# Optimization experiments

Hardware: AMD Instinct MI355X
Metric: run time of the kernel (lower is better)

The kernel has to match this reference:

```python
import jax, jax.numpy as jnp
import numpy as np

B, N, C, H, KH = 4, 4096, 1024, 16, 5
HD = C // H  # head dim = 64


def setup_inputs() -> dict:
    key = jax.random.key(0)
    ks = jax.random.split(key, 4)
    return {
        "x": jax.random.normal(ks[0], (B, N, C), jnp.float32),
        "qkv_w": jax.random.normal(ks[1], (3 * C, C), jnp.float32) * 0.02,
        "qkv_b": jnp.zeros((3 * C,), jnp.float32),
        "proj_w": jax.random.normal(ks[2], (C, C), jnp.float32) * 0.02,
        "proj_b": jnp.zeros((C,), jnp.float32),
        "pos_enc": jnp.zeros((1, C), jnp.float32),  # torch init: zeros
        "dwc_w": jax.random.normal(ks[3], (HD, 1, KH, KH), jnp.float32) * 0.05,
        "dwc_b": jnp.zeros((HD,), jnp.float32),
        "num_heads": H,
    }


def reference(x, qkv_w, qkv_b, proj_w, proj_b, pos_enc, dwc_w, dwc_b, num_heads):
    b, n, c = x.shape
    h = num_heads
    hd = c // h
    kh = dwc_w.shape[2]

    qkv = x @ qkv_w.T + qkv_b                     # (b, n, 3c)
    q, k, v = jnp.split(qkv, 3, axis=-1)          # each (b, n, c)
    k = k + pos_enc[:, :c]                        # broadcast (1, c)
    q = jax.nn.relu(q)
    k = jax.nn.relu(k)

    def to_heads(t):  # (b, n, c) -> (b*h, n, hd)
        return t.reshape(b, n, h, hd).transpose(0, 2, 1, 3).reshape(b * h, n, hd)

    q, k, v = to_heads(q), to_heads(k), to_heads(v)

    # linear attention in fp32 (inputs already fp32)
    z = 1.0 / (jnp.einsum('bic,bc->bi', q, k.sum(axis=1)) + 1e-6)   # (bh, n)
    kv = jnp.einsum('bjc,bjd->bcd', k, v)                           # (bh, hd, hd)
    out = jnp.einsum('bic,bcd->bid', q, kv) * z[:, :, None]         # (bh, n, hd)

    # depthwise 2D conv on v viewed as (bh, hd, n, 1), kernel (hd,1,kh,kh), pad kh//2
    fm = v.transpose(0, 2, 1)[..., None]                            # (bh, hd, n, 1)
    pad = kh // 2
    fm = jax.lax.conv_general_dilated(
        fm, dwc_w, window_strides=(1, 1),
        padding=((pad, pad), (pad, pad)),
        dimension_numbers=('NCHW', 'OIHW', 'NCHW'),
        feature_group_count=hd,
    ) + dwc_b[None, :, None, None]
    out = out + fm[..., 0].transpose(0, 2, 1)                       # (bh, n, hd)

    out = out.reshape(b, h, n, hd).transpose(0, 2, 1, 3).reshape(b, n, c)
    return out @ proj_w.T + proj_b
```

## Files before the change

### kernel.cpp

```cpp
#include <hip/hip_runtime.h>


#define BB   4
#define NN   4096
#define CDIM 1024
#define NH   16
#define HDIM 64
#define BH   64

typedef __attribute__((ext_vector_type(8))) short short8;
typedef __attribute__((ext_vector_type(4))) float f32x4;
typedef unsigned short u16;

__device__ __forceinline__ float b2f(short s) {
    union { unsigned u; float f; } c;
    c.u = ((unsigned)(unsigned short)s) << 16;
    return c.f;
}
__device__ __forceinline__ u16 f2b(float f) {
    unsigned u = __float_as_uint(f);
    return (u16)((u + 0x7fffu + ((u >> 16) & 1u)) >> 16);
}
__device__ __forceinline__ void gload16(const void* g, void* l) {
    __builtin_amdgcn_global_load_lds((const __attribute__((address_space(1))) void*)g,
                                     (__attribute__((address_space(3))) void*)l, 16, 0, 0);
}

__global__ __launch_bounds__(256) void k_fill_diag(float* __restrict__ out, int n, float val)
{
    int i = blockIdx.x * 256 + threadIdx.x;
    if (i < n) out[i] = val;
}

__global__ __launch_bounds__(256) void k_f32_to_bf16(const float* __restrict__ in,
                                                     u16* __restrict__ out, int n4)
{
    int i = blockIdx.x * 256 + threadIdx.x;
    if (i < n4) {
        float4 v = reinterpret_cast<const float4*>(in)[i];
        ushort4 o;
        o.x = f2b(v.x); o.y = f2b(v.y); o.z = f2b(v.z); o.w = f2b(v.w);
        reinterpret_cast<ushort4*>(out)[i] = o;
    }
}

#define GEMM256_8PH()                                                                    \
    const int t = threadIdx.x;                                                           \
    const int l = t & 63, w = t >> 6;                                                    \
    const int wr = w >> 2, wc = w & 3;                                                   \
    const int fr = l & 15;                                                               \
    const int physE  = ((l >> 4) ^ ((fr >> 1) & 3)) * 8;                                 \
    const int qa     = ((l & 3) ^ ((l >> 3) & 3)) * 8;                                   \
    const int aRow   = w * 16 + (l >> 2);                                                \
    const u16* gA0 = A  + (size_t)(brow + aRow) * 1024 + qa;                             \
    const u16* gB0 = Bw + (size_t)(bcol + aRow) * 1024 + qa;                             \
    char* ldsc = (char*)lds;                                                             \
    const int afBase = (wr * 128 + fr) * 32 + physE;                                     \
    const int bfBase = 16384 + (wc * 64 + fr) * 32 + physE;                              \
    f32x4 acc[8][4];                                                                     \
    _Pragma("unroll")                                                                    \
    for (int m = 0; m < 8; ++m)                                                          \
        _Pragma("unroll")                                                                \
        for (int n = 0; n < 4; ++n) acc[m][n] = (f32x4){0.f, 0.f, 0.f, 0.f};             \
    auto STG = [&](int kt, int kh, int isB) {                                            \
        const u16* g = (isB ? gB0 : gA0) + kt * 64 + kh * 32;                            \
        char* d = ldsc + (kt & 1) * 65536 + isB * 32768 + kh * 16384 + w * 1024 + l * 16;\
        gload16(g,          d);                                                          \
        gload16(g + 131072, d + 8192);                                                   \
    };                                                                                   \
    STG(0,0,0); STG(0,0,1); STG(0,1,0); STG(0,1,1); STG(1,0,0); STG(1,0,1);              \
    asm volatile("s_waitcnt vmcnt(4)" ::: "memory");                                     \
    __builtin_amdgcn_sched_barrier(0);                                                   \
    __builtin_amdgcn_s_barrier();                                                        \
    __builtin_amdgcn_sched_barrier(0);                                                   \
    _Pragma("unroll 1")                                                                  \
    for (int kt = 0; kt < 16; ++kt) {                                                    \
        const int B0 = (kt & 1) * 32768;                                                 \
        short8 af[4], bf[4];                                                             \
                                                               \
        _Pragma("unroll")                                                                \
        for (int m = 0; m < 4; ++m)                                                      \
            af[m] = *reinterpret_cast<const short8*>(&lds[B0 + afBase + m * 512]);       \
        _Pragma("unroll")                                                                \
        for (int n = 0; n < 4; ++n)                                                      \
            bf[n] = *reinterpret_cast<const short8*>(&lds[B0 + bfBase + n * 512]);       \
        if (kt + 1 < 16) STG(kt + 1, 1, 0);                                              \
        __builtin_amdgcn_sched_barrier(0);                                               \
        __builtin_amdgcn_s_barrier();                                                    \
        asm volatile("s_waitcnt lgkmcnt(0)" ::: "memory");                               \
        __builtin_amdgcn_sched_barrier(0);                                               \
        __builtin_amdgcn_s_setprio(1);                                                   \
        _Pragma("unroll")                                                                \
        for (int m = 0; m < 4; ++m)                                                      \
            _Pragma("unroll")                                                            \
            for (int n = 0; n < 4; ++n)                                                  \
                acc[m][n] = __builtin_amdgcn_mfma_f32_16x16x32_bf16(af[m], bf[n], acc[m][n], 0, 0, 0); \
        __builtin_amdgcn_s_setprio(0);                                                   \
        __builtin_amdgcn_sched_barrier(0);                                               \
        __builtin_amdgcn_s_barrier();                                                    \
        __builtin_amdgcn_sched_barrier(0);                                               \
                                                               \
        _Pragma("unroll")                                                                \
        for (int m = 0; m < 4; ++m)                                                      \
            af[m] = *reinterpret_cast<const short8*>(&lds[B0 + afBase + (m + 4) * 512]); \
        if (kt + 1 < 16) STG(kt + 1, 1, 1);                                              \
        __builtin_amdgcn_sched_barrier(0);                                               \
        __builtin_amdgcn_s_barrier();                                                    \
        asm volatile("s_waitcnt lgkmcnt(0)" ::: "memory");                               \
        __builtin_amdgcn_sched_barrier(0);                                               \
        __builtin_amdgcn_s_setprio(1);                                                   \
        _Pragma("unroll")                                                                \
        for (int m = 0; m < 4; ++m)                                                      \
            _Pragma("unroll")                                                            \
            for (int n = 0; n < 4; ++n)                                                  \
                acc[m + 4][n] = __builtin_amdgcn_mfma_f32_16x16x32_bf16(af[m], bf[n], acc[m + 4][n], 0, 0, 0); \
        __builtin_amdgcn_s_setprio(0);                                                   \
        __builtin_amdgcn_sched_barrier(0);                                               \
        __builtin_amdgcn_s_barrier();                                                    \
        __builtin_amdgcn_sched_barrier(0);                                               \
                                                               \
        _Pragma("unroll")                                                                \
        for (int m = 0; m < 4; ++m)                                                      \
            af[m] = *reinterpret_cast<const short8*>(&lds[B0 + 8192 + afBase + m * 512]);\
        _Pragma("unroll")                                                                \
        for (int n = 0; n < 4; ++n)                                                      \
            bf[n] = *reinterpret_cast<const short8*>(&lds[B0 + 8192 + bfBase + n * 512]);\
        if (kt + 2 < 16) STG(kt + 2, 0, 0);                                              \
        __builtin_amdgcn_sched_barrier(0);                                               \
        __builtin_amdgcn_s_barrier();                                                    \
        asm volatile("s_waitcnt lgkmcnt(0)" ::: "memory");                               \
        __builtin_amdgcn_sched_barrier(0);                                               \
        __builtin_amdgcn_s_setprio(1);                                                   \
        _Pragma("unroll")                                                                \
        for (int m = 0; m < 4; ++m)                                                      \
            _Pragma("unroll")                                                            \
            for (int n = 0; n < 4; ++n)                                                  \
                acc[m][n] = __builtin_amdgcn_mfma_f32_16x16x32_bf16(af[m], bf[n], acc[m][n], 0, 0, 0); \
        __builtin_amdgcn_s_setprio(0);                                                   \
        __builtin_amdgcn_sched_barrier(0);                                               \
        __builtin_amdgcn_s_barrier();                                                    \
        __builtin_amdgcn_sched_barrier(0);                                               \
                                                               \
        _Pragma("unroll")                                                                \
        for (int m = 0; m < 4; ++m)                                                      \
            af[m] = *reinterpret_cast<const short8*>(&lds[B0 + 8192 + afBase + (m + 4) * 512]); \
        if (kt + 2 < 16) STG(kt + 2, 0, 1);                                              \
        __builtin_amdgcn_sched_barrier(0);                                               \
        __builtin_amdgcn_s_barrier();                                                    \
        asm volatile("s_waitcnt lgkmcnt(0)" ::: "memory");                               \
        __builtin_amdgcn_sched_barrier(0);                                               \
        __builtin_amdgcn_s_setprio(1);                                                   \
        _Pragma("unroll")                                                                \
        for (int m = 0; m < 4; ++m)                                                      \
            _Pragma("unroll")                                                            \
            for (int n = 0; n < 4; ++n)                                                  \
                acc[m + 4][n] = __builtin_amdgcn_mfma_f32_16x16x32_bf16(af[m], bf[n], acc[m + 4][n], 0, 0, 0); \
        __builtin_amdgcn_s_setprio(0);                                                   \
        __builtin_amdgcn_sched_barrier(0);                                               \
        if (kt < 15) { asm volatile("s_waitcnt vmcnt(4)" ::: "memory"); }                \
        else         { asm volatile("s_waitcnt vmcnt(0)" ::: "memory"); }                \
        __builtin_amdgcn_sched_barrier(0);                                               \
        __builtin_amdgcn_s_barrier();                                                    \
        __builtin_amdgcn_sched_barrier(0);                                               \
    }

__global__ __launch_bounds__(512, 2) void k_gemm1_256(
    const u16* __restrict__ A,
    const u16* __restrict__ Bw,
    const float* __restrict__ bias, const float* __restrict__ pos_enc,
    u16* __restrict__ q, u16* __restrict__ kk_, u16* __restrict__ v)
{
    __shared__ u16 lds[65536];
    const int lid = blockIdx.y * 12 + blockIdx.x;
    const int swz = (lid & 7) * 96 + (lid >> 3);
    const int bcol = (swz % 12) * 256;
    const int brow = (swz / 12) * 256;

    GEMM256_8PH()

    const int part = bcol >> 10;
    u16* dst = (part == 0) ? q : (part == 1) ? kk_ : v;
    const int col_base = bcol + wc * 64 + fr;
    const int row_base = brow + wr * 128 + (l >> 4) * 4;
    #pragma unroll
    for (int n = 0; n < 4; ++n) {
        const int gc = col_base + n * 16;
        const int c  = gc & 1023;
        float bv = bias[gc];
        if (part == 1) bv += pos_enc[c];
        const int h = c >> 6, d = c & 63;
        #pragma unroll
        for (int m = 0; m < 8; ++m)
            #pragma unroll
            for (int j = 0; j < 4; ++j) {
                const int gr = row_base + m * 16 + j;
                const int b_ = gr >> 12, i_ = gr & 4095;
                float val = acc[m][n][j] + bv;
                if (part != 2) val = fmaxf(val, 0.f);
                dst[(size_t)((b_ * NH + h) * NN + i_) * HDIM + d] = f2b(val);
            }
    }
}

__global__ __launch_bounds__(512, 2) void k_gemm2_256(
    const u16* __restrict__ A,
    const u16* __restrict__ Bw,
    const float* __restrict__ bias, float* __restrict__ out)
{
    __shared__ u16 lds[65536];
    const int lid = blockIdx.y * 4 + blockIdx.x;
    const int swz = (lid & 7) * 32 + (lid >> 3);
    const int bcol = (swz % 4) * 256;
    const int brow = (swz / 4) * 256;

    GEMM256_8PH()

    const int col_base = bcol + wc * 64 + fr;
    const int row_base = brow + wr * 128 + (l >> 4) * 4;
    #pragma unroll
    for (int n = 0; n < 4; ++n) {
        const int gc = col_base + n * 16;
        const float bv = bias[gc];
        #pragma unroll
        for (int m = 0; m < 8; ++m)
            #pragma unroll
            for (int j = 0; j < 4; ++j) {
                const int gr = row_base + m * 16 + j;
                out[(size_t)gr * CDIM + gc] = acc[m][n][j] + bv;
            }
    }
}

__global__ __launch_bounds__(256) void k_kv_partial(
    const u16* __restrict__ k, const u16* __restrict__ v,
    float* __restrict__ part_kv, float* __restrict__ part_ks)
{
    __shared__ float ks[32 * 64];
    __shared__ float vs[32 * 64];
    const int bh = blockIdx.x;
    const int chunk = blockIdx.y;
    const int t = threadIdx.x;
    const int cg = t >> 4;
    const int dg = t & 15;
    const int lr = t >> 3;
    const int lc = (t & 7) * 8;
    const size_t base = (size_t)bh * NN * HDIM + (size_t)chunk * 1024 * HDIM;
    float acc[4][4] = {};
    float ksac[4] = {};
    for (int j0 = 0; j0 < 1024; j0 += 32) {
        short8 kr = *reinterpret_cast<const short8*>(&k[base + (size_t)(j0 + lr) * 64 + lc]);
        short8 vr = *reinterpret_cast<const short8*>(&v[base + (size_t)(j0 + lr) * 64 + lc]);
        __syncthreads();
        #pragma unroll
        for (int j = 0; j < 8; ++j) {
            ks[lr * 64 + lc + j] = b2f(kr[j]);
            vs[lr * 64 + lc + j] = b2f(vr[j]);
        }
        __syncthreads();
        #pragma unroll
        for (int j = 0; j < 32; ++j) {
            float4 k4 = *reinterpret_cast<const float4*>(&ks[j * 64 + cg * 4]);
            float4 v4 = *reinterpret_cast<const float4*>(&vs[j * 64 + dg * 4]);
            const float* kp = reinterpret_cast<const float*>(&k4);
            const float* vp = reinterpret_cast<const float*>(&v4);
            #pragma unroll
            for (int ii = 0; ii < 4; ++ii) {
                ksac[ii] += kp[ii];
                #pragma unroll
                for (int jj = 0; jj < 4; ++jj)
                    acc[ii][jj] += kp[ii] * vp[jj];
            }
        }
    }
    const int pb = (chunk * BH + bh);
    #pragma unroll
    for (int ii = 0; ii < 4; ++ii) {
        #pragma unroll
        for (int jj = 0; jj < 4; ++jj)
            part_kv[pb * 4096 + (cg * 4 + ii) * 64 + dg * 4 + jj] = acc[ii][jj];
        if (dg == 0) part_ks[pb * 64 + cg * 4 + ii] = ksac[ii];
    }
}

__global__ __launch_bounds__(256) void k_kv_reduce_t(
    const float* __restrict__ part_kv, const float* __restrict__ part_ks,
    u16* __restrict__ kvt)
{
    const int bh = blockIdx.x;
    const int t = threadIdx.x;
    u16* base = kvt + bh * 5120;
    #pragma unroll
    for (int r = 0; r < 16; ++r) {
        const int idx = r * 256 + t;
        const int c = idx >> 6, d = idx & 63;
        float s = 0.f;
        #pragma unroll
        for (int ch = 0; ch < 4; ++ch) s += part_kv[(ch * BH + bh) * 4096 + idx];
        base[d * 64 + c] = f2b(s);
    }
    if (t < 64) {
        float s = 0.f;
        #pragma unroll
        for (int ch = 0; ch < 4; ++ch) s += part_ks[(ch * BH + bh) * 64 + t];
        base[4096 + t] = f2b(s);
    }
    for (int z = t; z < 960; z += 256) base[4160 + z] = 0;
}

__global__ __launch_bounds__(256) void k_attn_mfma(
    const u16* __restrict__ q, const u16* __restrict__ v,
    const u16* __restrict__ kvt,
    const float* __restrict__ dwc_w, const float* __restrict__ dwc_b,
    u16* __restrict__ out2)
{
    __shared__ u16 att[4][64 * 68];
    const int t = threadIdx.x;
    const int l = t & 63, w = t >> 6;
    const int bh = blockIdx.x;
    const int tb = blockIdx.y * 256 + w * 64;
    const size_t hb = (size_t)bh * NN * HDIM;
    const u16* qb  = q + hb + (size_t)tb * HDIM;
    const u16* kvb = kvt + bh * 5120;

    const int fr = l & 15;
    const int kfrag = (l >> 4) * 8;

    short8 bfr[5][2];
    #pragma unroll
    for (int n = 0; n < 5; ++n)
        #pragma unroll
        for (int ks = 0; ks < 2; ++ks)
            bfr[n][ks] = *reinterpret_cast<const short8*>(&kvb[(n * 16 + fr) * 64 + ks * 32 + kfrag]);

    f32x4 acc[4][5];
    #pragma unroll
    for (int m = 0; m < 4; ++m)
        #pragma unroll
        for (int n = 0; n < 5; ++n) acc[m][n] = (f32x4){0.f, 0.f, 0.f, 0.f};

    #pragma unroll
    for (int m = 0; m < 4; ++m)
        #pragma unroll
        for (int ks = 0; ks < 2; ++ks) {
            short8 a = *reinterpret_cast<const short8*>(&qb[(m * 16 + fr) * 64 + ks * 32 + kfrag]);
            #pragma unroll
            for (int n = 0; n < 5; ++n)
                acc[m][n] = __builtin_amdgcn_mfma_f32_16x16x32_bf16(a, bfr[n][ks], acc[m][n], 0, 0, 0);
        }

    #pragma unroll
    for (int m = 0; m < 4; ++m)
        #pragma unroll
        for (int j = 0; j < 4; ++j) {
            const float den = __shfl(acc[m][4][j], l & 48);
            const float z = 1.f / (den + 1e-6f);
            const int row = m * 16 + (l >> 4) * 4 + j;
            #pragma unroll
            for (int n = 0; n < 4; ++n)
                att[w][row * 68 + fr + n * 16] = f2b(acc[m][n][j] * z);
        }
    __syncthreads();

    const int d = l;
    float w5[5];
    #pragma unroll
    for (int dh = 0; dh < 5; ++dh) w5[dh] = dwc_w[d * 25 + dh * 5 + 2];
    const float cbias = dwc_b[d];
    const int b_ = bh >> 4, h_ = bh & 15;
    u16* obase = out2 + (size_t)b_ * NN * CDIM + (size_t)h_ * 64 + d;
    float win[5];
    #pragma unroll
    for (int p = 0; p < 4; ++p) {
        const int src = tb - 2 + p;
        win[p] = (src >= 0 && src < NN) ? b2f(v[hb + (size_t)src * 64 + d]) : 0.f;
    }
    for (int it = 0; it < 64; ++it) {
        const int srcn = tb + it + 2;
        win[4] = (srcn < NN) ? b2f(v[hb + (size_t)srcn * 64 + d]) : 0.f;
        const float fm = cbias + w5[0] * win[0] + w5[1] * win[1] + w5[2] * win[2]
                               + w5[3] * win[3] + w5[4] * win[4];
        const float attn = b2f((short)att[w][it * 68 + d]);
        obase[(size_t)(tb + it) * CDIM] = f2b(attn + fm);
        win[0] = win[1]; win[1] = win[2]; win[2] = win[3]; win[3] = win[4];
    }
}

extern "C" void kernel_launch(void* const* d_in, const int* in_sizes, int n_in,
                              void* d_out, int out_size, void* d_ws, size_t ws_size,
                              hipStream_t stream)
{
    const float* x       = (const float*)d_in[0];
    const float* qkv_w   = (const float*)d_in[1];
    const float* qkv_b   = (const float*)d_in[2];
    const float* proj_w  = (const float*)d_in[3];
    const float* proj_b  = (const float*)d_in[4];
    const float* pos_enc = (const float*)d_in[5];
    const float* dwc_w   = (const float*)d_in[6];
    const float* dwc_b   = (const float*)d_in[7];

    const size_t QKV = 16777216;
    char* p = (char*)d_ws;
    u16* q_b    = (u16*)p;               p += QKV * 2;
    u16* k_b    = (u16*)p;               p += QKV * 2;
    u16* v_b    = (u16*)p;               p += QKV * 2;
    u16* x_b    = (u16*)p;               p += QKV * 2;
    u16* qkvw_b = (u16*)p;               p += (size_t)3145728 * 2;
    u16* projw_b= (u16*)p;               p += (size_t)1048576 * 2;
    float* part_kv = (float*)p;          p += (size_t)1048576 * 4;
    float* part_ks = (float*)p;          p += (size_t)16384 * 4;
    u16* kvt       = (u16*)p;            p += (size_t)(64 * 5120) * 2;
    const size_t need_bytes = (size_t)(p - (char*)d_ws);

    if (ws_size < need_bytes) {
        const float diag = 4096.0f + (float)(ws_size >> 20);
        k_fill_diag<<<(out_size + 255) / 256, 256, 0, stream>>>((float*)d_out, out_size, diag);
        return;
    }

    u16* out2 = k_b;
    float* out = (float*)d_out;

    k_f32_to_bf16<<<16384, 256, 0, stream>>>(x,      x_b,     4194304);
    k_f32_to_bf16<<< 3072, 256, 0, stream>>>(qkv_w,  qkvw_b,   786432);
    k_f32_to_bf16<<< 1024, 256, 0, stream>>>(proj_w, projw_b,  262144);

    k_gemm1_256  <<<dim3(12, 64), 512, 0, stream>>>(x_b, qkvw_b, qkv_b, pos_enc, q_b, k_b, v_b);
    k_kv_partial <<<dim3(64, 4),  256, 0, stream>>>(k_b, v_b, part_kv, part_ks);
    k_kv_reduce_t<<<64,           256, 0, stream>>>(part_kv, part_ks, kvt);
    k_attn_mfma  <<<dim3(64, 16), 256, 0, stream>>>(q_b, v_b, kvt, dwc_w, dwc_b, out2);
    k_gemm2_256  <<<dim3(4, 64),  512, 0, stream>>>(out2, projw_b, proj_b, out);
}
```

Measured before the change: 312.8 us.

## Stage GEMM1 epilogue through LDS, emit transposed K/V, compute KV with MFMA

The QKV GEMM epilogue now stages results in swizzled LDS, then writes Q and V with coalesced 16-byte stores and also writes transposed K and V (head-dim major) copies. The KV outer product and the K column sum are moved from scalar FP32 FMA loops onto bf16 MFMA, using a ones vector to produce the K sum. Partial results are reduced in LDS and then across chunks, giving a kvt layout that attention reads directly. This removes scattered 2-byte epilogue stores and slow scalar KV math. The cost is an extra transposed V write (more memory traffic and workspace) and a transposed-K layout of the KV result, whose orientation has to match what attention expects.

```diff
diff --git a/kernel.cpp b/kernel.cpp
--- a/kernel.cpp
+++ b/kernel.cpp
@@ -77,7 +77,6 @@
     for (int kt = 0; kt < 16; ++kt) {                                                    \
         const int B0 = (kt & 1) * 32768;                                                 \
         short8 af[4], bf[4];                                                             \
-                                                               \
         _Pragma("unroll")                                                                \
         for (int m = 0; m < 4; ++m)                                                      \
             af[m] = *reinterpret_cast<const short8*>(&lds[B0 + afBase + m * 512]);       \
@@ -99,7 +98,6 @@
         __builtin_amdgcn_sched_barrier(0);                                               \
         __builtin_amdgcn_s_barrier();                                                    \
         __builtin_amdgcn_sched_barrier(0);                                               \
-                                                               \
         _Pragma("unroll")                                                                \
         for (int m = 0; m < 4; ++m)                                                      \
             af[m] = *reinterpret_cast<const short8*>(&lds[B0 + afBase + (m + 4) * 512]); \
@@ -118,7 +116,6 @@
         __builtin_amdgcn_sched_barrier(0);                                               \
         __builtin_amdgcn_s_barrier();                                                    \
         __builtin_amdgcn_sched_barrier(0);                                               \
-                                                               \
         _Pragma("unroll")                                                                \
         for (int m = 0; m < 4; ++m)                                                      \
             af[m] = *reinterpret_cast<const short8*>(&lds[B0 + 8192 + afBase + m * 512]);\
@@ -140,7 +137,6 @@
         __builtin_amdgcn_sched_barrier(0);                                               \
         __builtin_amdgcn_s_barrier();                                                    \
         __builtin_amdgcn_sched_barrier(0);                                               \
-                                                               \
         _Pragma("unroll")                                                                \
         for (int m = 0; m < 4; ++m)                                                      \
             af[m] = *reinterpret_cast<const short8*>(&lds[B0 + 8192 + afBase + (m + 4) * 512]); \
@@ -168,7 +164,7 @@
     const u16* __restrict__ A,
     const u16* __restrict__ Bw,
     const float* __restrict__ bias, const float* __restrict__ pos_enc,
-    u16* __restrict__ q, u16* __restrict__ kk_, u16* __restrict__ v)
+    u16* __restrict__ q, u16* __restrict__ ktg, u16* __restrict__ v, u16* __restrict__ vtg)
 {
     __shared__ u16 lds[65536];
     const int lid = blockIdx.y * 12 + blockIdx.x;
@@ -179,32 +175,63 @@
     GEMM256_8PH()
 
     const int part = bcol >> 10;
-    u16* dst = (part == 0) ? q : (part == 1) ? kk_ : v;
-    const int col_base = bcol + wc * 64 + fr;
-    const int row_base = brow + wr * 128 + (l >> 4) * 4;
-    #pragma unroll
-    for (int n = 0; n < 4; ++n) {
-        const int gc = col_base + n * 16;
-        const int c  = gc & 1023;
-        float bv = bias[gc];
-        if (part == 1) bv += pos_enc[c];
-        const int h = c >> 6, d = c & 63;
-        #pragma unroll
-        for (int m = 0; m < 8; ++m)
-            #pragma unroll
-            for (int j = 0; j < 4; ++j) {
-                const int gr = row_base + m * 16 + j;
-                const int b_ = gr >> 12, i_ = gr & 4095;
-                float val = acc[m][n][j] + bv;
-                if (part != 2) val = fmaxf(val, 0.f);
-                dst[(size_t)((b_ * NH + h) * NN + i_) * HDIM + d] = f2b(val);
-            }
+    {
+        const int row_l = wr * 128 + (l >> 4) * 4;
+        const int col_l = wc * 64 + fr;
+        #pragma unroll
+        for (int n = 0; n < 4; ++n) {
+            const int col = col_l + n * 16;
+            const int gc = bcol + col;
+            const int c = gc & 1023;
+            float bv = bias[gc];
+            if (part == 1) bv += pos_enc[c];
+            const int cc = col >> 3, in = col & 7;
+            #pragma unroll
+            for (int m = 0; m < 8; ++m)
+                #pragma unroll
+                for (int j = 0; j < 4; ++j) {
+                    const int row = row_l + m * 16 + j;
+                    float val = acc[m][n][j] + bv;
+                    if (part != 2) val = fmaxf(val, 0.f);
+                    lds[row * 256 + ((cc ^ (row & 7)) << 3) + in] = f2b(val);
+                }
+        }
+    }
+    __syncthreads();
+    const int b_ = brow >> 12, i0 = brow & 4095;
+    if (part != 1) {
+        u16* dst = (part == 0) ? q : v;
+        #pragma unroll
+        for (int it = 0; it < 16; ++it) {
+            const int id = it * 512 + t;
+            const int row = id >> 5, cc = id & 31;
+            short8 val = *reinterpret_cast<const short8*>(&lds[row * 256 + ((cc ^ (row & 7)) << 3)]);
+            const int c2 = (bcol + cc * 8) & 1023;
+            const int h2 = c2 >> 6, d2 = c2 & 63;
+            *reinterpret_cast<short8*>(
+                &dst[((size_t)(b_ * NH + h2) * NN + i0 + row) * HDIM + d2]) = val;
+        }
+    }
+    if (part != 0) {
+        u16* dstT = (part == 1) ? ktg : vtg;
+        #pragma unroll
+        for (int it = 0; it < 16; ++it) {
+            const int id = it * 512 + t;
+            const int cl = id & 255, jc = id >> 8;
+            short8 vv;
+            #pragma unroll
+            for (int rr = 0; rr < 8; ++rr)
+                vv[rr] = (short)lds[(jc * 8 + rr) * 256 + (((cl >> 3) ^ rr) << 3) + (cl & 7)];
+            const int c2 = (bcol + cl) & 1023;
+            const int h2 = c2 >> 6, d2 = c2 & 63;
+            *reinterpret_cast<short8*>(
+                &dstT[((size_t)(b_ * NH + h2) * HDIM + d2) * NN + i0 + jc * 8]) = vv;
+        }
     }
 }
 
 __global__ __launch_bounds__(512, 2) void k_gemm2_256(
-    const u16* __restrict__ A,
-    const u16* __restrict__ Bw,
+    const u16* __restrict__ A, const u16* __restrict__ Bw,
     const float* __restrict__ bias, float* __restrict__ out)
 {
     __shared__ u16 lds[65536];
@@ -231,80 +258,70 @@
     }
 }
 
-__global__ __launch_bounds__(256) void k_kv_partial(
-    const u16* __restrict__ k, const u16* __restrict__ v,
-    float* __restrict__ part_kv, float* __restrict__ part_ks)
-{
-    __shared__ float ks[32 * 64];
-    __shared__ float vs[32 * 64];
-    const int bh = blockIdx.x;
-    const int chunk = blockIdx.y;
-    const int t = threadIdx.x;
-    const int cg = t >> 4;
-    const int dg = t & 15;
-    const int lr = t >> 3;
-    const int lc = (t & 7) * 8;
-    const size_t base = (size_t)bh * NN * HDIM + (size_t)chunk * 1024 * HDIM;
-    float acc[4][4] = {};
-    float ksac[4] = {};
-    for (int j0 = 0; j0 < 1024; j0 += 32) {
-        short8 kr = *reinterpret_cast<const short8*>(&k[base + (size_t)(j0 + lr) * 64 + lc]);
-        short8 vr = *reinterpret_cast<const short8*>(&v[base + (size_t)(j0 + lr) * 64 + lc]);
-        __syncthreads();
-        #pragma unroll
-        for (int j = 0; j < 8; ++j) {
-            ks[lr * 64 + lc + j] = b2f(kr[j]);
-            vs[lr * 64 + lc + j] = b2f(vr[j]);
-        }
-        __syncthreads();
-        #pragma unroll
-        for (int j = 0; j < 32; ++j) {
-            float4 k4 = *reinterpret_cast<const float4*>(&ks[j * 64 + cg * 4]);
-            float4 v4 = *reinterpret_cast<const float4*>(&vs[j * 64 + dg * 4]);
-            const float* kp = reinterpret_cast<const float*>(&k4);
-            const float* vp = reinterpret_cast<const float*>(&v4);
-            #pragma unroll
-            for (int ii = 0; ii < 4; ++ii) {
-                ksac[ii] += kp[ii];
-                #pragma unroll
-                for (int jj = 0; jj < 4; ++jj)
-                    acc[ii][jj] += kp[ii] * vp[jj];
-            }
-        }
-    }
-    const int pb = (chunk * BH + bh);
-    #pragma unroll
-    for (int ii = 0; ii < 4; ++ii) {
-        #pragma unroll
-        for (int jj = 0; jj < 4; ++jj)
-            part_kv[pb * 4096 + (cg * 4 + ii) * 64 + dg * 4 + jj] = acc[ii][jj];
-        if (dg == 0) part_ks[pb * 64 + cg * 4 + ii] = ksac[ii];
-    }
-}
-
-__global__ __launch_bounds__(256) void k_kv_reduce_t(
-    const float* __restrict__ part_kv, const float* __restrict__ part_ks,
-    u16* __restrict__ kvt)
-{
-    const int bh = blockIdx.x;
-    const int t = threadIdx.x;
+__global__ __launch_bounds__(256) void k_kv_mfma(
+    const u16* __restrict__ ktg, const u16* __restrict__ vtg,
+    float* __restrict__ part)
+{
+    __shared__ float red[4][5120];
+    const int t = threadIdx.x, l = t & 63, w = t >> 6;
+    const int bh = blockIdx.x, ch = blockIdx.y;
+    const u16* kb = ktg + (size_t)bh * HDIM * NN;
+    const u16* vb = vtg + (size_t)bh * HDIM * NN;
+    const int j0 = ch * 1024 + w * 256;
+    const int fr = l & 15, kf = (l >> 4) * 8;
+
+    f32x4 acc[5][4];
+    #pragma unroll
+    for (int m = 0; m < 5; ++m)
+        #pragma unroll
+        for (int n = 0; n < 4; ++n) acc[m][n] = (f32x4){0.f, 0.f, 0.f, 0.f};
+    short8 ones;
+    #pragma unroll
+    for (int i = 0; i < 8; ++i) ones[i] = (short)0x3F80;
+
+    for (int js = 0; js < 256; js += 32) {
+        const int jb = j0 + js + kf;
+        short8 a[4], b[4];
+        #pragma unroll
+        for (int m = 0; m < 4; ++m)
+            a[m] = *reinterpret_cast<const short8*>(&vb[(size_t)(m * 16 + fr) * NN + jb]);
+        #pragma unroll
+        for (int n = 0; n < 4; ++n)
+            b[n] = *reinterpret_cast<const short8*>(&kb[(size_t)(n * 16 + fr) * NN + jb]);
+        #pragma unroll
+        for (int m = 0; m < 4; ++m)
+            #pragma unroll
+            for (int n = 0; n < 4; ++n)
+                acc[m][n] = __builtin_amdgcn_mfma_f32_16x16x32_bf16(a[m], b[n], acc[m][n], 0, 0, 0);
+        #pragma unroll
+        for (int n = 0; n < 4; ++n)
+            acc[4][n] = __builtin_amdgcn_mfma_f32_16x16x32_bf16(ones, b[n], acc[4][n], 0, 0, 0);
+    }
+    #pragma unroll
+    for (int m = 0; m < 5; ++m)
+        #pragma unroll
+        for (int n = 0; n < 4; ++n)
+            #pragma unroll
+            for (int j = 0; j < 4; ++j)
+                red[w][(m * 16 + (l >> 4) * 4 + j) * 64 + fr + n * 16] = acc[m][n][j];
+    __syncthreads();
+    float* po = part + ((size_t)ch * BH + bh) * 5120;
+    for (int i = t; i < 5120; i += 256)
+        po[i] = red[0][i] + red[1][i] + red[2][i] + red[3][i];
+}
+
+__global__ __launch_bounds__(256) void k_kv_red(
+    const float* __restrict__ part, u16* __restrict__ kvt)
+{
+    const int bh = blockIdx.x, t = threadIdx.x;
     u16* base = kvt + bh * 5120;
-    #pragma unroll
-    for (int r = 0; r < 16; ++r) {
-        const int idx = r * 256 + t;
-        const int c = idx >> 6, d = idx & 63;
-        float s = 0.f;
-        #pragma unroll
-        for (int ch = 0; ch < 4; ++ch) s += part_kv[(ch * BH + bh) * 4096 + idx];
-        base[d * 64 + c] = f2b(s);
-    }
-    if (t < 64) {
-        float s = 0.f;
-        #pragma unroll
-        for (int ch = 0; ch < 4; ++ch) s += part_ks[(ch * BH + bh) * 64 + t];
-        base[4096 + t] = f2b(s);
-    }
-    for (int z = t; z < 960; z += 256) base[4160 + z] = 0;
+    for (int i = t; i < 5120; i += 256) {
+        float s = part[(size_t)(0 * BH + bh) * 5120 + i]
+                + part[(size_t)(1 * BH + bh) * 5120 + i]
+                + part[(size_t)(2 * BH + bh) * 5120 + i]
+                + part[(size_t)(3 * BH + bh) * 5120 + i];
+        base[i] = f2b(s);
+    }
 }
 
 __global__ __launch_bounds__(256) void k_attn_mfma(
@@ -401,14 +418,14 @@
     const size_t QKV = 16777216;
     char* p = (char*)d_ws;
     u16* q_b    = (u16*)p;               p += QKV * 2;
-    u16* k_b    = (u16*)p;               p += QKV * 2;
+    u16* ktg    = (u16*)p;               p += QKV * 2;
     u16* v_b    = (u16*)p;               p += QKV * 2;
+    u16* vtg    = (u16*)p;               p += QKV * 2;
     u16* x_b    = (u16*)p;               p += QKV * 2;
     u16* qkvw_b = (u16*)p;               p += (size_t)3145728 * 2;
     u16* projw_b= (u16*)p;               p += (size_t)1048576 * 2;
-    float* part_kv = (float*)p;          p += (size_t)1048576 * 4;
-    float* part_ks = (float*)p;          p += (size_t)16384 * 4;
-    u16* kvt       = (u16*)p;            p += (size_t)(64 * 5120) * 2;
+    float* part = (float*)p;             p += (size_t)4 * BH * 5120 * 4;
+    u16* kvt    = (u16*)p;               p += (size_t)(BH * 5120) * 2;
     const size_t need_bytes = (size_t)(p - (char*)d_ws);
 
     if (ws_size < need_bytes) {
@@ -417,16 +434,16 @@
         return;
     }
 
-    u16* out2 = k_b;
+    u16* out2 = ktg;
     float* out = (float*)d_out;
 
     k_f32_to_bf16<<<16384, 256, 0, stream>>>(x,      x_b,     4194304);
     k_f32_to_bf16<<< 3072, 256, 0, stream>>>(qkv_w,  qkvw_b,   786432);
     k_f32_to_bf16<<< 1024, 256, 0, stream>>>(proj_w, projw_b,  262144);
 
-    k_gemm1_256  <<<dim3(12, 64), 512, 0, stream>>>(x_b, qkvw_b, qkv_b, pos_enc, q_b, k_b, v_b);
-    k_kv_partial <<<dim3(64, 4),  256, 0, stream>>>(k_b, v_b, part_kv, part_ks);
-    k_kv_reduce_t<<<64,           256, 0, stream>>>(part_kv, part_ks, kvt);
-    k_attn_mfma  <<<dim3(64, 16), 256, 0, stream>>>(q_b, v_b, kvt, dwc_w, dwc_b, out2);
-    k_gemm2_256  <<<dim3(4, 64),  512, 0, stream>>>(out2, projw_b, proj_b, out);
-}
+    k_gemm1_256 <<<dim3(12, 64), 512, 0, stream>>>(x_b, qkvw_b, qkv_b, pos_enc, q_b, ktg, v_b, vtg);
+    k_kv_mfma   <<<dim3(64, 4),  256, 0, stream>>>(ktg, vtg, part);
+    k_kv_red    <<<64,           256, 0, stream>>>(part, kvt);
+    k_attn_mfma <<<dim3(64, 16), 256, 0, stream>>>(q_b, v_b, kvt, dwc_w, dwc_b, out2);
+    k_gemm2_256 <<<dim3(4, 64),  512, 0, stream>>>(out2, projw_b, proj_b, out);
+}
```

Measured after the change: 286.1 us. 8.5% less time.
